# Kernel optimization log

Hardware: AMD Instinct MI355X
Metric: run time of the kernel (lower is better)

The kernel has to match this reference:

```python
import jax, jax.numpy as jnp
import numpy as np

B, LQ, D, NH, NL, NP, DFFN = 16, 900, 256, 8, 4, 4, 2048
HD = D // NH
SHAPES = [(128, 128), (64, 64), (32, 32), (16, 16)]
LIN = sum(h * w for h, w in SHAPES)


def setup_inputs():
    ks = jax.random.split(jax.random.key(0), 24)
    p = lambda k, s: jax.random.normal(k, s, jnp.float32) * 0.02
    z = lambda s: jnp.zeros(s, jnp.float32)
    return {
        "queries": jax.random.normal(ks[0], (B, LQ, D), jnp.float32),
        "features": jax.random.normal(ks[1], (B, LIN, D), jnp.float32),
        "reference_points": jax.random.uniform(ks[2], (B, LQ, NL, 2), jnp.float32),
        "q_pos": jax.random.normal(ks[3], (B, LQ, D), jnp.float32),
        "in_proj_w": p(ks[4], (3 * D, D)), "in_proj_b": z((3 * D,)),
        "out_proj_w": p(ks[5], (D, D)), "out_proj_b": z((D,)),
        "value_proj_w": p(ks[6], (D, D)), "value_proj_b": z((D,)),
        "samp_w": p(ks[7], (NH * NL * NP * 2, D)),
        "samp_b": jax.random.uniform(ks[8], (NH * NL * NP * 2,), jnp.float32, -0.5, 0.5),
        "attw_w": p(ks[9], (NH * NL * NP, D)), "attw_b": z((NH * NL * NP,)),
        "msout_w": p(ks[10], (D, D)), "msout_b": z((D,)),
        "ffn_w1": p(ks[11], (DFFN, D)), "ffn_b1": z((DFFN,)),
        "ffn_w2": p(ks[12], (D, DFFN)), "ffn_b2": z((D,)),
        "ln1_g": jnp.ones((D,), jnp.float32), "ln1_b": z((D,)),
        "ln2_g": jnp.ones((D,), jnp.float32), "ln2_b": z((D,)),
        "ln3_g": jnp.ones((D,), jnp.float32), "ln3_b": z((D,)),
        "kv_spatial_shapes": np.array(SHAPES, np.int32),
        "level_start_index": np.concatenate([[0], np.cumsum([h * w for h, w in SHAPES])[:-1]]).astype(np.int32),
    }


def _ln(x, g, b, eps=1e-5):
    m = x.mean(-1, keepdims=True)
    v = ((x - m) ** 2).mean(-1, keepdims=True)
    return (x - m) * jax.lax.rsqrt(v + eps) * g + b


def _mha(q, k, v, wqkv, bqkv, wo, bo):
    wq, wk, wv = wqkv[:D], wqkv[D:2 * D], wqkv[2 * D:]
    bq, bk, bv = bqkv[:D], bqkv[D:2 * D], bqkv[2 * D:]
    qh = (q @ wq.T + bq).reshape(B, LQ, NH, HD)
    kh = (k @ wk.T + bk).reshape(B, LQ, NH, HD)
    vh = (v @ wv.T + bv).reshape(B, LQ, NH, HD)
    s = jnp.einsum("bqhd,bkhd->bhqk", qh, kh) / jnp.sqrt(jnp.float32(HD))
    a = jax.nn.softmax(s, axis=-1)
    o = jnp.einsum("bhqk,bkhd->bqhd", a, vh).reshape(B, LQ, D)
    return o @ wo.T + bo


def _ms_deform(value, loc, attw):
    # value (B,LIN,NH,HD); loc (B,LQ,NH,NL,NP,2) normalized; attw (B,LQ,NH,NL,NP)
    out = jnp.zeros((B, LQ, NH, HD), jnp.float32)
    start = 0
    for l, (hl, wl) in enumerate(SHAPES):
        v = value[:, start:start + hl * wl].transpose(0, 2, 1, 3)  # (B,NH,hl*wl,HD)
        g = loc[:, :, :, l]  # (B,LQ,NH,NP,2)
        # grid_sample align_corners=False pixel coords
        x = g[..., 0] * wl - 0.5
        y = g[..., 1] * hl - 0.5
        x0 = jnp.floor(x); y0 = jnp.floor(y)
        fx = x - x0; fy = y - y0
        x0 = x0.astype(jnp.int32); y0 = y0.astype(jnp.int32)
        acc = jnp.zeros((B, LQ, NH, NP, HD), jnp.float32)
        for dy, wy in ((0, 1.0 - fy), (1, fy)):
            for dx, wx in ((0, 1.0 - fx), (1, fx)):
                xi = x0 + dx; yi = y0 + dy
                valid = (xi >= 0) & (xi < wl) & (yi >= 0) & (yi < hl)
                idx = jnp.clip(yi, 0, hl - 1) * wl + jnp.clip(xi, 0, wl - 1)
                idx = idx.transpose(0, 2, 1, 3).reshape(B, NH, LQ * NP)
                s = jnp.take_along_axis(v, idx[..., None], axis=2)
                s = s.reshape(B, NH, LQ, NP, HD).transpose(0, 2, 1, 3, 4)
                w = jnp.where(valid, wy * wx, 0.0)  # zero-padding outside
                acc = acc + s * w[..., None]
        out = out + (acc * attw[:, :, :, l, :, None]).sum(3)
        start += hl * wl
    return out.reshape(B, LQ, D)


def reference(queries, features, reference_points, q_pos, in_proj_w, in_proj_b, out_proj_w, out_proj_b, value_proj_w, value_proj_b, samp_w, samp_b, attw_w, attw_b, msout_w, msout_b, ffn_w1, ffn_b1, ffn_w2, ffn_b2, ln1_g, ln1_b, ln2_g, ln2_b, ln3_g, ln3_b, kv_spatial_shapes, level_start_index):
    qk = queries + q_pos
    x = _ln(queries + _mha(qk, qk, queries, in_proj_w, in_proj_b, out_proj_w, out_proj_b), ln1_g, ln1_b)
    # deformable multi-scale cross attention
    q2 = x + q_pos
    value = (features @ value_proj_w.T + value_proj_b).reshape(B, LIN, NH, HD)
    off = (q2 @ samp_w.T + samp_b).reshape(B, LQ, NH, NL, NP, 2)
    attw = jax.nn.softmax((q2 @ attw_w.T + attw_b).reshape(B, LQ, NH, NL * NP), axis=-1).reshape(B, LQ, NH, NL, NP)
    norm = jnp.stack([jnp.asarray(kv_spatial_shapes)[:, 1], jnp.asarray(kv_spatial_shapes)[:, 0]], -1).astype(jnp.float32)  # (NL,2)=(W,H)
    loc = reference_points[:, :, None, :, None, :] + off / norm[None, None, None, :, None, :]
    ms = _ms_deform(value, loc, attw) @ msout_w.T + msout_b
    x = _ln(x + ms, ln2_g, ln2_b)
    ffn = jax.nn.relu(x @ ffn_w1.T + ffn_b1) @ ffn_w2.T + ffn_b2
    return _ln(x + ffn, ln3_g, ln3_b)
```

## Files before the change

kernel.cpp:

```cpp
#include <hip/hip_runtime.h>
#include <hip/hip_bf16.h>
#include <math.h>

#define B_    16
#define LQ_   900
#define D_    256
#define NH_   8
#define HD_   32
#define NL_   4
#define NP_   4
#define DFFN_ 2048
#define LIN_  21760

typedef unsigned short u16;
typedef __attribute__((ext_vector_type(8))) short bf16x8;
typedef __attribute__((ext_vector_type(4))) float f32x4;

__device__ __forceinline__ short f2bf(float f) {
    unsigned u = __float_as_uint(f);
    u += 0x7fffu + ((u >> 16) & 1u);
    return (short)(u >> 16);
}
__device__ __forceinline__ float bf2f(u16 u) {
    return __uint_as_float(((unsigned)u) << 16);
}

#define WOFF_INPROJ  0
#define WOFF_OUTPROJ 196608
#define WOFF_VALPROJ 262144
#define WOFF_SAMP    327680
#define WOFF_ATTW    393216
#define WOFF_MSOUT   425984
#define WOFF_FFN1    491520
#define WOFF_FFN2    1015808
#define WTOTAL       1540096

__global__ __launch_bounds__(256) void wprep_kernel(const float* __restrict__ s0,
                                                    const float* __restrict__ s1,
                                                    const float* __restrict__ s2,
                                                    const float* __restrict__ s3,
                                                    const float* __restrict__ s4,
                                                    const float* __restrict__ s5,
                                                    const float* __restrict__ s6,
                                                    const float* __restrict__ s7,
                                                    u16* __restrict__ Wb) {
    int i8 = (blockIdx.x * 256 + threadIdx.x) * 8;
    if (i8 >= WTOTAL) return;
    const float* src; int rel;
    if      (i8 < WOFF_OUTPROJ) { src = s0; rel = i8; }
    else if (i8 < WOFF_VALPROJ) { src = s1; rel = i8 - WOFF_OUTPROJ; }
    else if (i8 < WOFF_SAMP)    { src = s2; rel = i8 - WOFF_VALPROJ; }
    else if (i8 < WOFF_ATTW)    { src = s3; rel = i8 - WOFF_SAMP; }
    else if (i8 < WOFF_MSOUT)   { src = s4; rel = i8 - WOFF_ATTW; }
    else if (i8 < WOFF_FFN1)    { src = s5; rel = i8 - WOFF_MSOUT; }
    else if (i8 < WOFF_FFN2)    { src = s6; rel = i8 - WOFF_FFN1; }
    else                        { src = s7; rel = i8 - WOFF_FFN2; }
    float4 v0 = *(const float4*)(src + rel);
    float4 v1 = *(const float4*)(src + rel + 4);
    short o[8];
    o[0] = f2bf(v0.x); o[1] = f2bf(v0.y); o[2] = f2bf(v0.z); o[3] = f2bf(v0.w);
    o[4] = f2bf(v1.x); o[5] = f2bf(v1.y); o[6] = f2bf(v1.z); o[7] = f2bf(v1.w);
    *(bf16x8*)(Wb + i8) = *(bf16x8*)o;
}

#define BOFF_INPROJ  0
#define BOFF_OUTPROJ 768
#define BOFF_VALPROJ 1024
#define BOFF_SAMPATT 1280
#define BOFF_MSOUT   1664
#define BOFF_FFN1    1920
#define BOFF_FFN2    3968
#define BTOTAL       4224

__global__ __launch_bounds__(256) void bprep_kernel(const float* __restrict__ b0,
                                                    const float* __restrict__ b1,
                                                    const float* __restrict__ b2,
                                                    const float* __restrict__ b3,
                                                    const float* __restrict__ b4,
                                                    const float* __restrict__ b5,
                                                    const float* __restrict__ b6,
                                                    const float* __restrict__ b7,
                                                    float* __restrict__ Bb) {
    int i = blockIdx.x * 256 + threadIdx.x;
    if (i >= BTOTAL) return;
    const float* s; int rel;
    if      (i < BOFF_OUTPROJ) { s = b0; rel = i; }
    else if (i < BOFF_VALPROJ) { s = b1; rel = i - BOFF_OUTPROJ; }
    else if (i < BOFF_SAMPATT) { s = b2; rel = i - BOFF_VALPROJ; }
    else if (i < 1536)         { s = b3; rel = i - BOFF_SAMPATT; }
    else if (i < BOFF_MSOUT)   { s = b4; rel = i - 1536; }
    else if (i < BOFF_FFN1)    { s = b5; rel = i - BOFF_MSOUT; }
    else if (i < BOFF_FFN2)    { s = b6; rel = i - BOFF_FFN1; }
    else                       { s = b7; rel = i - BOFF_FFN2; }
    Bb[i] = s[rel];
}

__global__ __launch_bounds__(256) void add_bf16_kernel(const float* __restrict__ a,
                                                       const float* __restrict__ b,
                                                       u16* __restrict__ osum,
                                                       u16* __restrict__ oa,
                                                       size_t n4) {
    size_t i = (size_t)blockIdx.x * blockDim.x + threadIdx.x;
    if (i >= n4) return;
    float4 x = ((const float4*)a)[i];
    float4 y = ((const float4*)b)[i];
    ushort4 s;
    s.x = (u16)f2bf(x.x + y.x); s.y = (u16)f2bf(x.y + y.y);
    s.z = (u16)f2bf(x.z + y.z); s.w = (u16)f2bf(x.w + y.w);
    ((ushort4*)osum)[i] = s;
    if (oa) {
        ushort4 q;
        q.x = (u16)f2bf(x.x); q.y = (u16)f2bf(x.y);
        q.z = (u16)f2bf(x.z); q.w = (u16)f2bf(x.w);
        ((ushort4*)oa)[i] = q;
    }
}

#define LDK 40
template <typename TA, typename TC>
__global__ __launch_bounds__(256) void gemm3_kernel(const TA* __restrict__ A,
                                                    const u16* __restrict__ W,
                                                    const float* __restrict__ bias,
                                                    const float* __restrict__ res,
                                                    TC* __restrict__ C,
                                                    int M, int N, int K, int relu) {
    __shared__ __align__(16) u16 As[2][128 * LDK];
    __shared__ __align__(16) u16 Bs[2][128 * LDK];

    const int n0 = blockIdx.x * 128;
    const int m0 = blockIdx.y * 128;
    const int t  = threadIdx.x;
    const int srow = t >> 1;
    const int scol = (t & 1) << 4;
    const int lane = t & 63;
    const int lr   = lane & 15;
    const int kg   = lane >> 4;
    const int wid  = t >> 6;
    const int wr   = wid >> 1;
    const int wc   = wid & 1;

    f32x4 acc[4][4] = {};

    const int  nk  = K >> 5;
    const int  gm  = m0 + srow;
    const bool mok = (gm < M);

    const float* af32 = (const float*)A + (size_t)(mok ? gm : 0) * K + scol;
    const u16*   ab16 = (const u16*)A + (size_t)(mok ? gm : 0) * K + scol;
    const u16*   wp   = W + (size_t)(n0 + srow) * K + scol;

    float4 af0[4], af1[4];
    bf16x8 ab0[2], ab1[2];
    bf16x8 wf0[2], wf1[2];
    if (!mok) {
        #pragma unroll
        for (int q = 0; q < 4; ++q) af0[q] = af1[q] = make_float4(0.f, 0.f, 0.f, 0.f);
        #pragma unroll
        for (int q = 0; q < 8; ++q) { ab0[0][q] = 0; ab0[1][q] = 0; ab1[0][q] = 0; ab1[1][q] = 0; }
    }

#define GLOAD_A_F(afX, kt_) do { if (mok) { \
        _Pragma("unroll") for (int q = 0; q < 4; ++q) afX[q] = *(const float4*)(af32 + ((kt_) << 5) + q * 4); } } while (0)
#define GLOAD_A_B(abX, kt_) do { if (mok) { \
        abX[0] = *(const bf16x8*)(ab16 + ((kt_) << 5)); \
        abX[1] = *(const bf16x8*)(ab16 + ((kt_) << 5) + 8); } } while (0)
#define GLOAD_W(wfX, kt_) do { \
        wfX[0] = *(const bf16x8*)(wp + ((kt_) << 5)); \
        wfX[1] = *(const bf16x8*)(wp + ((kt_) << 5) + 8); } while (0)

#define DSWRITE(bufI, afX, abX, wfX) do { \
        if constexpr (sizeof(TA) == 4) { \
            short tmp[16]; \
            _Pragma("unroll") for (int q = 0; q < 4; ++q) { \
                tmp[q * 4 + 0] = f2bf(afX[q].x); tmp[q * 4 + 1] = f2bf(afX[q].y); \
                tmp[q * 4 + 2] = f2bf(afX[q].z); tmp[q * 4 + 3] = f2bf(afX[q].w); } \
            *(bf16x8*)&As[bufI][srow * LDK + scol]     = *(bf16x8*)tmp; \
            *(bf16x8*)&As[bufI][srow * LDK + scol + 8] = *(bf16x8*)(tmp + 8); \
        } else { \
            *(bf16x8*)&As[bufI][srow * LDK + scol]     = abX[0]; \
            *(bf16x8*)&As[bufI][srow * LDK + scol + 8] = abX[1]; } \
        *(bf16x8*)&Bs[bufI][srow * LDK + scol]     = wfX[0]; \
        *(bf16x8*)&Bs[bufI][srow * LDK + scol + 8] = wfX[1]; } while (0)

    auto domfma = [&](const u16* bufA, const u16* bufB) {
        const u16* pA = bufA + (wr * 64 + lr) * LDK + kg * 8;
        const u16* pB = bufB + (wc * 64 + lr) * LDK + kg * 8;
        bf16x8 a[4], b[4];
        #pragma unroll
        for (int i = 0; i < 4; ++i) a[i] = *(const bf16x8*)(pA + i * 16 * LDK);
        #pragma unroll
        for (int j = 0; j < 4; ++j) b[j] = *(const bf16x8*)(pB + j * 16 * LDK);
        #pragma unroll
        for (int i = 0; i < 4; ++i)
            #pragma unroll
            for (int j = 0; j < 4; ++j)
                acc[i][j] = __builtin_amdgcn_mfma_f32_16x16x32_bf16(a[i], b[j], acc[i][j], 0, 0, 0);
    };

    if constexpr (sizeof(TA) == 4) { GLOAD_A_F(af0, 0); GLOAD_A_F(af1, 1); }
    else                           { GLOAD_A_B(ab0, 0); GLOAD_A_B(ab1, 1); }
    GLOAD_W(wf0, 0); GLOAD_W(wf1, 1);

    int kt = 0;
    while (true) {
        DSWRITE(0, af0, ab0, wf0);
        if (kt + 2 < nk) {
            if constexpr (sizeof(TA) == 4) GLOAD_A_F(af0, kt + 2); else GLOAD_A_B(ab0, kt + 2);
            GLOAD_W(wf0, kt + 2);
        }
        __syncthreads();
        domfma(&As[0][0], &Bs[0][0]);
        if (++kt >= nk) break;
        DSWRITE(1, af1, ab1, wf1);
        if (kt + 2 < nk) {
            if constexpr (sizeof(TA) == 4) GLOAD_A_F(af1, kt + 2); else GLOAD_A_B(ab1, kt + 2);
            GLOAD_W(wf1, kt + 2);
        }
        __syncthreads();
        domfma(&As[1][0], &Bs[1][0]);
        if (++kt >= nk) break;
    }
#undef GLOAD_A_F
#undef GLOAD_A_B
#undef GLOAD_W
#undef DSWRITE

    #pragma unroll
    for (int i = 0; i < 4; ++i) {
        #pragma unroll
        for (int j = 0; j < 4; ++j) {
            const int n = n0 + wc * 64 + j * 16 + lr;
            const float bn = bias[n];
            #pragma unroll
            for (int r = 0; r < 4; ++r) {
                const int m = m0 + wr * 64 + i * 16 + kg * 4 + r;
                if (m < M) {
                    float v = acc[i][j][r] + bn;
                    if (res)  v += res[(size_t)m * N + n];
                    if (relu) v = fmaxf(v, 0.f);
                    if constexpr (sizeof(TC) == 4) C[(size_t)m * N + n] = v;
                    else                           C[(size_t)m * N + n] = (TC)(u16)f2bf(v);
                }
            }
        }
    }
}

#define LDA2 40
#define LDP  72
__global__ __launch_bounds__(256) void attn_mfma_kernel(const u16* __restrict__ QKg,
                                                        const u16* __restrict__ Vg,
                                                        u16* __restrict__ Og) {
    __shared__ __align__(16) u16 Ks[64 * LDA2];
    __shared__ __align__(16) u16 Vs[64 * LDA2];
    __shared__ __align__(16) u16 Ps[4][16 * LDP];

    const int qt = blockIdx.x, h = blockIdx.y, b = blockIdx.z;
    const int t  = threadIdx.x;
    const int wq = t >> 6;
    const int lane = t & 63;
    const int l15  = lane & 15;
    const int g    = lane >> 4;
    const int q0   = qt * 64;

    const int srow = t >> 2;
    const int sd   = (t & 3) * 8;

    int qrow = q0 + wq * 16 + l15;
    if (qrow > LQ_ - 1) qrow = LQ_ - 1;
    const bf16x8 qfrag = *(const bf16x8*)(QKg + ((size_t)(b * LQ_) + qrow) * 512 + h * HD_ + g * 8);

    float m_i = -1e30f, l_i = 0.f;
    f32x4 o_acc[2] = {};
    const float scale = 0.17677669529663687f;

    for (int k0 = 0; k0 < 960; k0 += 64) {
        {
            int kr = k0 + srow;
            bf16x8 kv, vv;
            if (kr < LQ_) {
                kv = *(const bf16x8*)(QKg + ((size_t)(b * LQ_) + kr) * 512 + 256 + h * HD_ + sd);
                vv = *(const bf16x8*)(Vg + ((size_t)(b * LQ_) + kr) * D_ + h * HD_ + sd);
            } else {
                #pragma unroll
                for (int j = 0; j < 8; ++j) { kv[j] = 0; vv[j] = 0; }
            }
            *(bf16x8*)&Ks[srow * LDA2 + sd] = kv;
            *(bf16x8*)&Vs[srow * LDA2 + sd] = vv;
        }
        __syncthreads();

        float p[4][4];
        float tmax = -1e30f;
        #pragma unroll
        for (int kt = 0; kt < 4; ++kt) {
            bf16x8 af = *(const bf16x8*)&Ks[(kt * 16 + l15) * LDA2 + g * 8];
            f32x4 c = {0.f, 0.f, 0.f, 0.f};
            c = __builtin_amdgcn_mfma_f32_16x16x32_bf16(af, qfrag, c, 0, 0, 0);
            #pragma unroll
            for (int r = 0; r < 4; ++r) {
                int kglob = k0 + kt * 16 + g * 4 + r;
                float s = (kglob < LQ_) ? c[r] * scale : -1e30f;
                p[kt][r] = s;
                tmax = fmaxf(tmax, s);
            }
        }
        tmax = fmaxf(tmax, __shfl_xor(tmax, 16));
        tmax = fmaxf(tmax, __shfl_xor(tmax, 32));
        float newm = fmaxf(m_i, tmax);
        float corr = __expf(m_i - newm);
        float rs = 0.f;
        #pragma unroll
        for (int kt = 0; kt < 4; ++kt) {
            #pragma unroll
            for (int r = 0; r < 4; ++r) {
                float e = __expf(p[kt][r] - newm);
                p[kt][r] = e;
                rs += e;
            }
            ushort4 pk;
            pk.x = (u16)f2bf(p[kt][0]);
            pk.y = (u16)f2bf(p[kt][1]);
            pk.z = (u16)f2bf(p[kt][2]);
            pk.w = (u16)f2bf(p[kt][3]);
            *(ushort4*)&Ps[wq][l15 * LDP + kt * 16 + g * 4] = pk;
        }
        rs += __shfl_xor(rs, 16);
        rs += __shfl_xor(rs, 32);
        l_i = l_i * corr + rs;
        m_i = newm;

        #pragma unroll
        for (int r = 0; r < 4; ++r) {
            float cq = __shfl(corr, g * 4 + r);
            o_acc[0][r] *= cq;
            o_acc[1][r] *= cq;
        }

        #pragma unroll
        for (int c = 0; c < 2; ++c) {
            bf16x8 pa = *(const bf16x8*)&Ps[wq][l15 * LDP + c * 32 + g * 8];
            #pragma unroll
            for (int nt = 0; nt < 2; ++nt) {
                short vv[8];
                #pragma unroll
                for (int j = 0; j < 8; ++j)
                    vv[j] = (short)Vs[(c * 32 + g * 8 + j) * LDA2 + nt * 16 + l15];
                o_acc[nt] = __builtin_amdgcn_mfma_f32_16x16x32_bf16(pa, *(bf16x8*)vv, o_acc[nt], 0, 0, 0);
            }
        }
        __syncthreads();
    }

    float il = 1.f / l_i;
    #pragma unroll
    for (int r = 0; r < 4; ++r) {
        float ilq = __shfl(il, g * 4 + r);
        int q = q0 + wq * 16 + g * 4 + r;
        if (q < LQ_) {
            u16* dst = Og + ((size_t)(b * LQ_) + q) * D_ + h * HD_ + l15;
            dst[0]  = (u16)f2bf(o_acc[0][r] * ilq);
            dst[16] = (u16)f2bf(o_acc[1][r] * ilq);
        }
    }
}

__global__ __launch_bounds__(256) void ln_kernel(const float* __restrict__ X,
                                                 const float* __restrict__ g,
                                                 const float* __restrict__ bb,
                                                 float* __restrict__ Y,
                                                 u16* __restrict__ Yb, int M) {
    int row  = blockIdx.x * 4 + (threadIdx.x >> 6);
    int lane = threadIdx.x & 63;
    if (row >= M) return;
    const float* x = X + (size_t)row * D_;
    float4 v = *(const float4*)(x + lane * 4);
    float s = v.x + v.y + v.z + v.w;
    #pragma unroll
    for (int o = 32; o >= 1; o >>= 1) s += __shfl_xor(s, o);
    float mean = s * (1.f / D_);
    float dx0 = v.x - mean, dx1 = v.y - mean, dx2 = v.z - mean, dx3 = v.w - mean;
    float ss = dx0 * dx0 + dx1 * dx1 + dx2 * dx2 + dx3 * dx3;
    #pragma unroll
    for (int o = 32; o >= 1; o >>= 1) ss += __shfl_xor(ss, o);
    float rstd = rsqrtf(ss * (1.f / D_) + 1e-5f);
    float4 gv = *(const float4*)(g + lane * 4);
    float4 bv = *(const float4*)(bb + lane * 4);
    float4 out;
    out.x = dx0 * rstd * gv.x + bv.x;
    out.y = dx1 * rstd * gv.y + bv.y;
    out.z = dx2 * rstd * gv.z + bv.z;
    out.w = dx3 * rstd * gv.w + bv.w;
    *(float4*)(Y + (size_t)row * D_ + lane * 4) = out;
    if (Yb) {
        ushort4 ob;
        ob.x = (u16)f2bf(out.x); ob.y = (u16)f2bf(out.y);
        ob.z = (u16)f2bf(out.z); ob.w = (u16)f2bf(out.w);
        *(ushort4*)(Yb + (size_t)row * D_ + lane * 4) = ob;
    }
}

__global__ __launch_bounds__(256) void softmax16v_kernel(const float* __restrict__ X,
                                                         float* __restrict__ Y,
                                                         int rows) {
    int r = blockIdx.x * blockDim.x + threadIdx.x;
    if (r >= rows) return;
    const float* x = X + (size_t)(r >> 3) * 384 + 256 + (r & 7) * 16;
    float m = -1e30f;
    #pragma unroll
    for (int i = 0; i < 16; ++i) m = fmaxf(m, x[i]);
    float e[16], s = 0.f;
    #pragma unroll
    for (int i = 0; i < 16; ++i) { e[i] = expf(x[i] - m); s += e[i]; }
    float inv = 1.f / s;
    float* y = Y + (size_t)r * 16;
    #pragma unroll
    for (int i = 0; i < 16; ++i) y[i] = e[i] * inv;
}

__global__ __launch_bounds__(256) void msdeform2_kernel(const u16* __restrict__ value,
                                                        const float* __restrict__ ref,
                                                        const float* __restrict__ off,
                                                        const float* __restrict__ attw,
                                                        u16* __restrict__ out) {
    const int levH[4] = {128, 64, 32, 16};
    const int levW[4] = {128, 64, 32, 16};
    const int levS[4] = {0, 16384, 20480, 21504};

    int gid = blockIdx.x * 256 + threadIdx.x;
    int d8  = gid & 3;
    int bqh = gid >> 2;
    int h   = bqh & (NH_ - 1);
    int bq  = bqh >> 3;
    int b   = bq / LQ_;

    const float* refp = ref  + (size_t)bq * NL_ * 2;
    const float* offp = off  + (size_t)bq * 384 + h * 32;
    const float* awp  = attw + (size_t)bq * 128 + h * 16;
    const u16* vbase  = value + (size_t)b * LIN_ * D_ + h * HD_ + d8 * 8;

    float acc[8] = {};
    #pragma unroll
    for (int l = 0; l < NL_; ++l) {
        float rx = refp[l * 2 + 0], ry = refp[l * 2 + 1];
        const int wl = levW[l], hl = levH[l];
        const u16* vlev = vbase + (size_t)levS[l] * D_;
        #pragma unroll
        for (int p = 0; p < NP_; ++p) {
            float ox = offp[(l * NP_ + p) * 2 + 0];
            float oy = offp[(l * NP_ + p) * 2 + 1];
            float x = rx * wl + ox - 0.5f;
            float y = ry * hl + oy - 0.5f;
            float x0f = floorf(x), y0f = floorf(y);
            float fx = x - x0f, fy = y - y0f;
            int x0 = (int)x0f, y0 = (int)y0f;
            float aw = awp[l * NP_ + p];
            #pragma unroll
            for (int dy = 0; dy < 2; ++dy) {
                int   yi = y0 + dy;
                float wy = dy ? fy : 1.f - fy;
                bool  vy = (yi >= 0) && (yi < hl);
                int   yc = min(max(yi, 0), hl - 1);
                #pragma unroll
                for (int dx = 0; dx < 2; ++dx) {
                    int   xi = x0 + dx;
                    float wx = dx ? fx : 1.f - fx;
                    bool  vx = (xi >= 0) && (xi < wl);
                    int   xc = min(max(xi, 0), wl - 1);
                    float w  = (vx && vy) ? aw * wy * wx : 0.f;
                    bf16x8 v = *(const bf16x8*)(vlev + (size_t)(yc * wl + xc) * D_);
                    #pragma unroll
                    for (int j = 0; j < 8; ++j)
                        acc[j] += w * bf2f((u16)v[j]);
                }
            }
        }
    }
    short o[8];
    #pragma unroll
    for (int j = 0; j < 8; ++j) o[j] = f2bf(acc[j]);
    *(bf16x8*)(out + (size_t)bq * D_ + h * HD_ + d8 * 8) = *(bf16x8*)o;
}

extern "C" void kernel_launch(void* const* d_in, const int* in_sizes, int n_in,
                              void* d_out, int out_size, void* d_ws, size_t ws_size,
                              hipStream_t stream) {
    const float* queries      = (const float*)d_in[0];
    const float* features     = (const float*)d_in[1];
    const float* refpts       = (const float*)d_in[2];
    const float* q_pos        = (const float*)d_in[3];
    const float* in_proj_w    = (const float*)d_in[4];
    const float* in_proj_b    = (const float*)d_in[5];
    const float* out_proj_w   = (const float*)d_in[6];
    const float* out_proj_b   = (const float*)d_in[7];
    const float* value_proj_w = (const float*)d_in[8];
    const float* value_proj_b = (const float*)d_in[9];
    const float* samp_w       = (const float*)d_in[10];
    const float* samp_b       = (const float*)d_in[11];
    const float* attw_w       = (const float*)d_in[12];
    const float* attw_b       = (const float*)d_in[13];
    const float* msout_w      = (const float*)d_in[14];
    const float* msout_b      = (const float*)d_in[15];
    const float* ffn_w1       = (const float*)d_in[16];
    const float* ffn_b1       = (const float*)d_in[17];
    const float* ffn_w2       = (const float*)d_in[18];
    const float* ffn_b2       = (const float*)d_in[19];
    const float* ln1_g        = (const float*)d_in[20];
    const float* ln1_b        = (const float*)d_in[21];
    const float* ln2_g        = (const float*)d_in[22];
    const float* ln2_b        = (const float*)d_in[23];
    const float* ln3_g        = (const float*)d_in[24];
    const float* ln3_b        = (const float*)d_in[25];

    float* ws = (float*)d_ws;
    const size_t NQ = (size_t)B_ * LQ_ * D_;
    float* bufB = ws;
    float* bufC = ws + 3 * NQ / 2;
    float* bufF = bufC + NQ;
    float* bufD = bufF + NQ;
    u16* U    = (u16*)(bufD + NQ);
    u16* qkb  = U;
    u16* qb   = U + NQ;
    u16* q2b  = U + 2 * NQ;
    u16* QKb  = U + 3 * NQ;
    u16* Vb   = U + 5 * NQ;
    u16* Ob   = U + 6 * NQ;
    u16* MSb  = U + 7 * NQ;
    u16* LN2b = U + 8 * NQ;
    u16* VALb = U + 9 * NQ;
    u16* H1b  = VALb + (size_t)B_ * LIN_ * D_;
    u16* Wb   = H1b + (size_t)B_ * LQ_ * DFFN_;
    float* Bb = (float*)(Wb + WTOTAL);

    const int M = B_ * LQ_;
    const int GY = 113;

    wprep_kernel<<<752, 256, 0, stream>>>(in_proj_w, out_proj_w, value_proj_w, samp_w,
                                          attw_w, msout_w, ffn_w1, ffn_w2, Wb);
    bprep_kernel<<<17, 256, 0, stream>>>(in_proj_b, out_proj_b, value_proj_b, samp_b,
                                         attw_b, msout_b, ffn_b1, ffn_b2, Bb);

    add_bf16_kernel<<<3600, 256, 0, stream>>>(queries, q_pos, qkb, qb, NQ / 4);

    gemm3_kernel<u16, u16><<<dim3(4, GY), 256, 0, stream>>>(qkb, Wb + WOFF_INPROJ, Bb + BOFF_INPROJ, nullptr, QKb, M, 512, 256, 0);
    gemm3_kernel<u16, u16><<<dim3(2, GY), 256, 0, stream>>>(qb, Wb + WOFF_INPROJ + 131072, Bb + BOFF_INPROJ + 512, nullptr, Vb, M, 256, 256, 0);

    attn_mfma_kernel<<<dim3(15, NH_, B_), 256, 0, stream>>>(QKb, Vb, Ob);

    gemm3_kernel<u16, float><<<dim3(2, GY), 256, 0, stream>>>(Ob, Wb + WOFF_OUTPROJ, Bb + BOFF_OUTPROJ, queries, bufC, M, 256, 256, 0);
    ln_kernel<<<3600, 256, 0, stream>>>(bufC, ln1_g, ln1_b, bufF, nullptr, M);

    add_bf16_kernel<<<3600, 256, 0, stream>>>(bufF, q_pos, q2b, nullptr, NQ / 4);

    gemm3_kernel<float, u16><<<dim3(2, 2720), 256, 0, stream>>>(features, Wb + WOFF_VALPROJ, Bb + BOFF_VALPROJ, nullptr, VALb, B_ * LIN_, 256, 256, 0);

    gemm3_kernel<u16, float><<<dim3(3, GY), 256, 0, stream>>>(q2b, Wb + WOFF_SAMP, Bb + BOFF_SAMPATT, nullptr, bufB, M, 384, 256, 0);

    softmax16v_kernel<<<450, 256, 0, stream>>>(bufB, bufD, B_ * LQ_ * NH_);

    msdeform2_kernel<<<1800, 256, 0, stream>>>(VALb, refpts, bufB, bufD, MSb);

    gemm3_kernel<u16, float><<<dim3(2, GY), 256, 0, stream>>>(MSb, Wb + WOFF_MSOUT, Bb + BOFF_MSOUT, bufF, bufC, M, 256, 256, 0);
    ln_kernel<<<3600, 256, 0, stream>>>(bufC, ln2_g, ln2_b, bufD, LN2b, M);

    gemm3_kernel<u16, u16><<<dim3(16, GY), 256, 0, stream>>>(LN2b, Wb + WOFF_FFN1, Bb + BOFF_FFN1, nullptr, H1b, M, 2048, 256, 1);

    gemm3_kernel<u16, float><<<dim3(2, GY), 256, 0, stream>>>(H1b, Wb + WOFF_FFN2, Bb + BOFF_FFN2, bufD, bufC, M, 256, 2048, 0);
    ln_kernel<<<3600, 256, 0, stream>>>(bufC, ln3_g, ln3_b, (float*)d_out, nullptr, M);
}
```

Measured before the change: 1.095 ms.

## Use 512-thread GEMM blocks with 8 waves and single-stage register prefetch

The shared GEMM kernel now runs with 512 threads (8 waves in a 2x4 grid) on the same 128x128 tile, so each wave holds a 64x32 accumulator instead of 64x64. The register prefetch depth drops from two k-tiles to one, and each thread stages 8 elements instead of 16. The aim is to cut per-thread register use and add waves to hide latency. In exchange, the LDS A fragments are read by more waves and less global load latency is hidden per thread.

```diff
diff --git a/kernel.cpp b/kernel.cpp
--- a/kernel.cpp
+++ b/kernel.cpp
@@ -118,7 +118,7 @@
 
 #define LDK 40
 template <typename TA, typename TC>
-__global__ __launch_bounds__(256) void gemm3_kernel(const TA* __restrict__ A,
+__global__ __launch_bounds__(512) void gemm4_kernel(const TA* __restrict__ A,
                                                     const u16* __restrict__ W,
                                                     const float* __restrict__ bias,
                                                     const float* __restrict__ res,
@@ -130,16 +130,16 @@
     const int n0 = blockIdx.x * 128;
     const int m0 = blockIdx.y * 128;
     const int t  = threadIdx.x;
-    const int srow = t >> 1;
-    const int scol = (t & 1) << 4;
+    const int srow = t >> 2;
+    const int scol = (t & 3) << 3;
     const int lane = t & 63;
     const int lr   = lane & 15;
     const int kg   = lane >> 4;
     const int wid  = t >> 6;
-    const int wr   = wid >> 1;
-    const int wc   = wid & 1;
-
-    f32x4 acc[4][4] = {};
+    const int wr   = wid >> 2;
+    const int wc   = wid & 3;
+
+    f32x4 acc[4][2] = {};
 
     const int  nk  = K >> 5;
     const int  gm  = m0 + srow;
@@ -149,87 +149,67 @@
     const u16*   ab16 = (const u16*)A + (size_t)(mok ? gm : 0) * K + scol;
     const u16*   wp   = W + (size_t)(n0 + srow) * K + scol;
 
-    float4 af0[4], af1[4];
-    bf16x8 ab0[2], ab1[2];
-    bf16x8 wf0[2], wf1[2];
+    float4 af[2];
+    bf16x8 ab;
+    bf16x8 wf;
     if (!mok) {
-        #pragma unroll
-        for (int q = 0; q < 4; ++q) af0[q] = af1[q] = make_float4(0.f, 0.f, 0.f, 0.f);
-        #pragma unroll
-        for (int q = 0; q < 8; ++q) { ab0[0][q] = 0; ab0[1][q] = 0; ab1[0][q] = 0; ab1[1][q] = 0; }
-    }
-
-#define GLOAD_A_F(afX, kt_) do { if (mok) { \
-        _Pragma("unroll") for (int q = 0; q < 4; ++q) afX[q] = *(const float4*)(af32 + ((kt_) << 5) + q * 4); } } while (0)
-#define GLOAD_A_B(abX, kt_) do { if (mok) { \
-        abX[0] = *(const bf16x8*)(ab16 + ((kt_) << 5)); \
-        abX[1] = *(const bf16x8*)(ab16 + ((kt_) << 5) + 8); } } while (0)
-#define GLOAD_W(wfX, kt_) do { \
-        wfX[0] = *(const bf16x8*)(wp + ((kt_) << 5)); \
-        wfX[1] = *(const bf16x8*)(wp + ((kt_) << 5) + 8); } while (0)
-
-#define DSWRITE(bufI, afX, abX, wfX) do { \
-        if constexpr (sizeof(TA) == 4) { \
-            short tmp[16]; \
-            _Pragma("unroll") for (int q = 0; q < 4; ++q) { \
-                tmp[q * 4 + 0] = f2bf(afX[q].x); tmp[q * 4 + 1] = f2bf(afX[q].y); \
-                tmp[q * 4 + 2] = f2bf(afX[q].z); tmp[q * 4 + 3] = f2bf(afX[q].w); } \
-            *(bf16x8*)&As[bufI][srow * LDK + scol]     = *(bf16x8*)tmp; \
-            *(bf16x8*)&As[bufI][srow * LDK + scol + 8] = *(bf16x8*)(tmp + 8); \
-        } else { \
-            *(bf16x8*)&As[bufI][srow * LDK + scol]     = abX[0]; \
-            *(bf16x8*)&As[bufI][srow * LDK + scol + 8] = abX[1]; } \
-        *(bf16x8*)&Bs[bufI][srow * LDK + scol]     = wfX[0]; \
-        *(bf16x8*)&Bs[bufI][srow * LDK + scol + 8] = wfX[1]; } while (0)
-
-    auto domfma = [&](const u16* bufA, const u16* bufB) {
-        const u16* pA = bufA + (wr * 64 + lr) * LDK + kg * 8;
-        const u16* pB = bufB + (wc * 64 + lr) * LDK + kg * 8;
-        bf16x8 a[4], b[4];
+        af[0] = af[1] = make_float4(0.f, 0.f, 0.f, 0.f);
+        #pragma unroll
+        for (int q = 0; q < 8; ++q) ab[q] = 0;
+    }
+
+    if constexpr (sizeof(TA) == 4) {
+        if (mok) { af[0] = *(const float4*)af32; af[1] = *(const float4*)(af32 + 4); }
+    } else {
+        if (mok) ab = *(const bf16x8*)ab16;
+    }
+    wf = *(const bf16x8*)wp;
+
+    for (int kt = 0; kt < nk; ++kt) {
+        const int cur = kt & 1;
+        if constexpr (sizeof(TA) == 4) {
+            short tmp[8];
+            tmp[0] = f2bf(af[0].x); tmp[1] = f2bf(af[0].y);
+            tmp[2] = f2bf(af[0].z); tmp[3] = f2bf(af[0].w);
+            tmp[4] = f2bf(af[1].x); tmp[5] = f2bf(af[1].y);
+            tmp[6] = f2bf(af[1].z); tmp[7] = f2bf(af[1].w);
+            *(bf16x8*)&As[cur][srow * LDK + scol] = *(bf16x8*)tmp;
+        } else {
+            *(bf16x8*)&As[cur][srow * LDK + scol] = ab;
+        }
+        *(bf16x8*)&Bs[cur][srow * LDK + scol] = wf;
+
+        if (kt + 1 < nk) {
+            const int k1 = (kt + 1) << 5;
+            if constexpr (sizeof(TA) == 4) {
+                if (mok) { af[0] = *(const float4*)(af32 + k1); af[1] = *(const float4*)(af32 + k1 + 4); }
+            } else {
+                if (mok) ab = *(const bf16x8*)(ab16 + k1);
+            }
+            wf = *(const bf16x8*)(wp + k1);
+        }
+
+        __syncthreads();
+
+        const u16* pA = &As[cur][(wr * 64 + lr) * LDK + kg * 8];
+        const u16* pB = &Bs[cur][(wc * 32 + lr) * LDK + kg * 8];
+        bf16x8 a[4], b[2];
         #pragma unroll
         for (int i = 0; i < 4; ++i) a[i] = *(const bf16x8*)(pA + i * 16 * LDK);
         #pragma unroll
-        for (int j = 0; j < 4; ++j) b[j] = *(const bf16x8*)(pB + j * 16 * LDK);
+        for (int j = 0; j < 2; ++j) b[j] = *(const bf16x8*)(pB + j * 16 * LDK);
         #pragma unroll
         for (int i = 0; i < 4; ++i)
             #pragma unroll
-            for (int j = 0; j < 4; ++j)
+            for (int j = 0; j < 2; ++j)
                 acc[i][j] = __builtin_amdgcn_mfma_f32_16x16x32_bf16(a[i], b[j], acc[i][j], 0, 0, 0);
-    };
-
-    if constexpr (sizeof(TA) == 4) { GLOAD_A_F(af0, 0); GLOAD_A_F(af1, 1); }
-    else                           { GLOAD_A_B(ab0, 0); GLOAD_A_B(ab1, 1); }
-    GLOAD_W(wf0, 0); GLOAD_W(wf1, 1);
-
-    int kt = 0;
-    while (true) {
-        DSWRITE(0, af0, ab0, wf0);
-        if (kt + 2 < nk) {
-            if constexpr (sizeof(TA) == 4) GLOAD_A_F(af0, kt + 2); else GLOAD_A_B(ab0, kt + 2);
-            GLOAD_W(wf0, kt + 2);
-        }
-        __syncthreads();
-        domfma(&As[0][0], &Bs[0][0]);
-        if (++kt >= nk) break;
-        DSWRITE(1, af1, ab1, wf1);
-        if (kt + 2 < nk) {
-            if constexpr (sizeof(TA) == 4) GLOAD_A_F(af1, kt + 2); else GLOAD_A_B(ab1, kt + 2);
-            GLOAD_W(wf1, kt + 2);
-        }
-        __syncthreads();
-        domfma(&As[1][0], &Bs[1][0]);
-        if (++kt >= nk) break;
-    }
-#undef GLOAD_A_F
-#undef GLOAD_A_B
-#undef GLOAD_W
-#undef DSWRITE
+    }
 
     #pragma unroll
     for (int i = 0; i < 4; ++i) {
         #pragma unroll
-        for (int j = 0; j < 4; ++j) {
-            const int n = n0 + wc * 64 + j * 16 + lr;
+        for (int j = 0; j < 2; ++j) {
+            const int n = n0 + wc * 32 + j * 16 + lr;
             const float bn = bias[n];
             #pragma unroll
             for (int r = 0; r < 4; ++r) {
@@ -542,29 +522,29 @@
 
     add_bf16_kernel<<<3600, 256, 0, stream>>>(queries, q_pos, qkb, qb, NQ / 4);
 
-    gemm3_kernel<u16, u16><<<dim3(4, GY), 256, 0, stream>>>(qkb, Wb + WOFF_INPROJ, Bb + BOFF_INPROJ, nullptr, QKb, M, 512, 256, 0);
-    gemm3_kernel<u16, u16><<<dim3(2, GY), 256, 0, stream>>>(qb, Wb + WOFF_INPROJ + 131072, Bb + BOFF_INPROJ + 512, nullptr, Vb, M, 256, 256, 0);
+    gemm4_kernel<u16, u16><<<dim3(4, GY), 512, 0, stream>>>(qkb, Wb + WOFF_INPROJ, Bb + BOFF_INPROJ, nullptr, QKb, M, 512, 256, 0);
+    gemm4_kernel<u16, u16><<<dim3(2, GY), 512, 0, stream>>>(qb, Wb + WOFF_INPROJ + 131072, Bb + BOFF_INPROJ + 512, nullptr, Vb, M, 256, 256, 0);
 
     attn_mfma_kernel<<<dim3(15, NH_, B_), 256, 0, stream>>>(QKb, Vb, Ob);
 
-    gemm3_kernel<u16, float><<<dim3(2, GY), 256, 0, stream>>>(Ob, Wb + WOFF_OUTPROJ, Bb + BOFF_OUTPROJ, queries, bufC, M, 256, 256, 0);
+    gemm4_kernel<u16, float><<<dim3(2, GY), 512, 0, stream>>>(Ob, Wb + WOFF_OUTPROJ, Bb + BOFF_OUTPROJ, queries, bufC, M, 256, 256, 0);
     ln_kernel<<<3600, 256, 0, stream>>>(bufC, ln1_g, ln1_b, bufF, nullptr, M);
 
     add_bf16_kernel<<<3600, 256, 0, stream>>>(bufF, q_pos, q2b, nullptr, NQ / 4);
 
-    gemm3_kernel<float, u16><<<dim3(2, 2720), 256, 0, stream>>>(features, Wb + WOFF_VALPROJ, Bb + BOFF_VALPROJ, nullptr, VALb, B_ * LIN_, 256, 256, 0);
-
-    gemm3_kernel<u16, float><<<dim3(3, GY), 256, 0, stream>>>(q2b, Wb + WOFF_SAMP, Bb + BOFF_SAMPATT, nullptr, bufB, M, 384, 256, 0);
+    gemm4_kernel<float, u16><<<dim3(2, 2720), 512, 0, stream>>>(features, Wb + WOFF_VALPROJ, Bb + BOFF_VALPROJ, nullptr, VALb, B_ * LIN_, 256, 256, 0);
+
+    gemm4_kernel<u16, float><<<dim3(3, GY), 512, 0, stream>>>(q2b, Wb + WOFF_SAMP, Bb + BOFF_SAMPATT, nullptr, bufB, M, 384, 256, 0);
 
     softmax16v_kernel<<<450, 256, 0, stream>>>(bufB, bufD, B_ * LQ_ * NH_);
 
     msdeform2_kernel<<<1800, 256, 0, stream>>>(VALb, refpts, bufB, bufD, MSb);
 
-    gemm3_kernel<u16, float><<<dim3(2, GY), 256, 0, stream>>>(MSb, Wb + WOFF_MSOUT, Bb + BOFF_MSOUT, bufF, bufC, M, 256, 256, 0);
+    gemm4_kernel<u16, float><<<dim3(2, GY), 512, 0, stream>>>(MSb, Wb + WOFF_MSOUT, Bb + BOFF_MSOUT, bufF, bufC, M, 256, 256, 0);
     ln_kernel<<<3600, 256, 0, stream>>>(bufC, ln2_g, ln2_b, bufD, LN2b, M);
 
-    gemm3_kernel<u16, u16><<<dim3(16, GY), 256, 0, stream>>>(LN2b, Wb + WOFF_FFN1, Bb + BOFF_FFN1, nullptr, H1b, M, 2048, 256, 1);
-
-    gemm3_kernel<u16, float><<<dim3(2, GY), 256, 0, stream>>>(H1b, Wb + WOFF_FFN2, Bb + BOFF_FFN2, bufD, bufC, M, 256, 2048, 0);
+    gemm4_kernel<u16, u16><<<dim3(16, GY), 512, 0, stream>>>(LN2b, Wb + WOFF_FFN1, Bb + BOFF_FFN1, nullptr, H1b, M, 2048, 256, 1);
+
+    gemm4_kernel<u16, float><<<dim3(2, GY), 512, 0, stream>>>(H1b, Wb + WOFF_FFN2, Bb + BOFF_FFN2, bufD, bufC, M, 256, 2048, 0);
     ln_kernel<<<3600, 256, 0, stream>>>(bufC, ln3_g, ln3_b, (float*)d_out, nullptr, M);
 }
```

Result: faster. 965.5 us (-11.8%).
